# Optimization experiments

Measured on AMD Instinct MI355X. Metric: run time of the kernel, lower is better.

The kernel has to match this reference:

```python
import jax, jax.numpy as jnp
import numpy as np

N, E, D_IN, D_OUT, R, B = 50000, 800000, 64, 64, 10, 4

def setup_inputs() -> dict:
    key = jax.random.key(0)
    ks = jax.random.split(key, 8)
    feat = jax.random.normal(ks[0], (N, D_IN), jnp.float32)
    src = jax.random.randint(ks[1], (E,), 0, N)
    dst = jax.random.randint(ks[2], (E,), 0, N)
    etype = jax.random.randint(ks[3], (E,), 0, R)
    norm = jax.random.uniform(ks[4], (E,), jnp.float32)
    weight = jax.random.normal(ks[5], (B, D_IN, D_OUT), jnp.float32) * 0.1
    w_comp = jax.random.normal(ks[6], (R, B), jnp.float32) * 0.1
    self_loop_weight = jax.random.normal(ks[7], (D_IN, D_OUT), jnp.float32) * 0.1
    return dict(feat=feat, src=src, dst=dst, etype=etype, norm=norm,
                weight=weight, w_comp=w_comp, self_loop_weight=self_loop_weight)

def reference(feat, src, dst, etype, norm, weight, w_comp, self_loop_weight):
    # Basis decomposition: per-relation weight W_r = sum_b w_comp[r,b] * weight[b]
    W = jnp.einsum('rb,bio->rio', w_comp, weight)            # [R, D_in, D_out]
    # Transform all nodes under every relation (R is small), then gather per edge.
    # This avoids materializing an [E, D_in, D_out] per-edge weight tensor.
    xr = jnp.einsum('ni,rio->rno', feat, W)                  # [R, N, D_out]
    msg = xr[etype, src] * norm[:, None]                     # [E, D_out]
    # Scatter-aggregate messages into destination nodes (DGL sum aggregator).
    agg = jax.ops.segment_sum(msg, dst, num_segments=N)      # [N, D_out]
    # SumAggregator adds curr_emb = dst_feat @ self_loop_weight to the msg sum.
    h = feat @ self_loop_weight + agg                        # [N, D_out]
    return jax.nn.relu(h)
```

## Files before the change

### kernel.cpp

```cpp
#include <hip/hip_runtime.h>
#include <hip/hip_bf16.h>
#include <stdint.h>

#define NN 50000
#define EE 800000
#define DD 64
#define RR 10
#define BB 4
#define NPAD 50176
#define NBKT 391
#define TBLK 4301
#define BBLK 196
#define PADCAP 8192
#define FCAP 4096

using u16 = unsigned short;
using u32 = unsigned int;

typedef short v8s __attribute__((ext_vector_type(8)));
typedef float v4f __attribute__((ext_vector_type(4)));

__device__ __forceinline__ u32 f2bf_rn(float x) {
    u32 u = __float_as_uint(x);
    return (u + 0x7FFFu + ((u >> 16) & 1u)) >> 16;
}
__device__ __forceinline__ u32 pack2bf(float a, float b) {
    return f2bf_rn(a) | (f2bf_rn(b) << 16);
}

__global__ __launch_bounds__(256, 2)
void k_big(const float* __restrict__ feat,
           const float* __restrict__ weight,
           const float* __restrict__ w_comp,
           const float* __restrict__ self_w,
           const int* __restrict__ src, const int* __restrict__ dst,
           const int* __restrict__ etype, const float* __restrict__ norm,
           int* __restrict__ bcur, int* __restrict__ flag,
           uint2* __restrict__ rec,
           u16* __restrict__ xr, float* __restrict__ out,
           int nbin, int tb_off, int cap) {
    __shared__ __align__(16) char smem[34816];
    const int t = threadIdx.x;

    if ((int)blockIdx.x < nbin) {
        int* lh  = (int*)smem;
        int* gb  = lh + 392;
        int* lcc = gb + 392;
        const int ebase = (int)blockIdx.x * 4096;
        for (int b = t; b < 392; b += 256) { lh[b] = 0; lcc[b] = 0; }
        __syncthreads();
        #pragma unroll 4
        for (int j = 0; j < 16; ++j) {
            int e = ebase + t + 256 * j;
            if (e < EE) atomicAdd(&lh[dst[e] >> 7], 1);
        }
        __syncthreads();
        for (int b = t; b < 392; b += 256) {
            int c = lh[b];
            gb[b] = c ? atomicAdd(&bcur[b], c) : 0;
        }
        __syncthreads();
        #pragma unroll 4
        for (int j = 0; j < 16; ++j) {
            int e = ebase + t + 256 * j;
            if (e < EE) {
                int d = dst[e];
                int b = d >> 7;
                int p = atomicAdd(&lcc[b], 1);
                u32 w0 = (u32)src[e] | ((u32)etype[e] << 16) | ((u32)(d & 127) << 20);
                if (cap) {
                    int il = gb[b] + p;
                    if (il < cap)
                        rec[(size_t)b * cap + il] = make_uint2(w0, __float_as_uint(norm[e]));
                    else
                        atomicOr(&flag[b], 2);
                } else {
                    rec[gb[b] + p] = make_uint2(w0, __float_as_uint(norm[e]));
                }
            }
        }
        return;
    }

    u16*   sWt = (u16*)smem;
    u16*   sFb = (u16*)(smem + 9216);
    float* sD  = (float*)smem;

    const int tb = (int)blockIdx.x - nbin + tb_off;
    const int r = tb / 391;
    const int nbase = (tb % 391) * 128;

    if (r < RR) {
        const float c0 = w_comp[r * BB + 0];
        const float c1 = w_comp[r * BB + 1];
        const float c2 = w_comp[r * BB + 2];
        const float c3 = w_comp[r * BB + 3];
        #pragma unroll
        for (int qq = 0; qq < 16; ++qq) {
            int idx = t + 256 * qq;
            int n = idx & 63, k = idx >> 6;
            float v = c0 * weight[k * 64 + n] + c1 * weight[4096 + k * 64 + n] +
                      c2 * weight[8192 + k * 64 + n] + c3 * weight[12288 + k * 64 + n];
            sWt[n * 72 + k] = (u16)f2bf_rn(v);
        }
    } else {
        #pragma unroll
        for (int qq = 0; qq < 16; ++qq) {
            int idx = t + 256 * qq;
            int n = idx & 63, k = idx >> 6;
            sWt[n * 72 + k] = (u16)f2bf_rn(self_w[k * 64 + n]);
        }
    }

    #pragma unroll
    for (int qq = 0; qq < 8; ++qq) {
        int f4 = qq * 256 + t;
        int nl = f4 >> 4;
        int ic = (f4 & 15) << 2;
        int n = nbase + nl;
        float4 v = make_float4(0.f, 0.f, 0.f, 0.f);
        if (n < NN) v = reinterpret_cast<const float4*>(feat)[(size_t)n * 16 + (f4 & 15)];
        *reinterpret_cast<uint2*>(&sFb[nl * 72 + ic]) =
            make_uint2(pack2bf(v.x, v.y), pack2bf(v.z, v.w));
    }
    __syncthreads();

    const int wv = t >> 6;
    const int L = t & 63;
    const int q = L >> 4;
    const int c = L & 15;

    v8s bf[4][2];
    #pragma unroll
    for (int nt = 0; nt < 4; ++nt)
        #pragma unroll
        for (int kh = 0; kh < 2; ++kh)
            bf[nt][kh] = *reinterpret_cast<const v8s*>(&sWt[(nt * 16 + c) * 72 + kh * 32 + q * 8]);

    v8s af[2][2];
    #pragma unroll
    for (int mt = 0; mt < 2; ++mt) {
        int row = wv * 32 + mt * 16 + c;
        #pragma unroll
        for (int kh = 0; kh < 2; ++kh)
            af[mt][kh] = *reinterpret_cast<const v8s*>(&sFb[row * 72 + kh * 32 + q * 8]);
    }
    __syncthreads();

    v4f acc[2][4];
    #pragma unroll
    for (int mt = 0; mt < 2; ++mt)
        #pragma unroll
        for (int nt = 0; nt < 4; ++nt) {
            acc[mt][nt] = (v4f)(0.f);
            #pragma unroll
            for (int kh = 0; kh < 2; ++kh)
                acc[mt][nt] = __builtin_amdgcn_mfma_f32_16x16x32_bf16(
                    af[mt][kh], bf[nt][kh], acc[mt][nt], 0, 0, 0);
        }

    #pragma unroll
    for (int mt = 0; mt < 2; ++mt) {
        int mrow = wv * 32 + mt * 16 + q * 4;
        #pragma unroll
        for (int nt = 0; nt < 4; ++nt)
            #pragma unroll
            for (int rg = 0; rg < 4; ++rg)
                sD[(mrow + rg) * 68 + nt * 16 + c] = acc[mt][nt][rg];
    }
    __syncthreads();

    const int row = t >> 1;
    const int cb = (t & 1) * 32;
    const int g = nbase + row;
    if (g < NN) {
        const float* sp = &sD[row * 68 + cb];
        if (r < RR) {
            u16* dp = xr + ((size_t)r * NN + g) * DD + cb;
            #pragma unroll
            for (int j = 0; j < 4; ++j) {
                float4 f0 = *reinterpret_cast<const float4*>(sp + j * 8);
                float4 f1 = *reinterpret_cast<const float4*>(sp + j * 8 + 4);
                uint4 o;
                o.x = pack2bf(f0.x, f0.y);
                o.y = pack2bf(f0.z, f0.w);
                o.z = pack2bf(f1.x, f1.y);
                o.w = pack2bf(f1.z, f1.w);
                *reinterpret_cast<uint4*>(dp + j * 8) = o;
            }
        } else {
            float* dp = out + (size_t)g * DD + cb;
            #pragma unroll
            for (int j = 0; j < 8; ++j)
                *reinterpret_cast<float4*>(dp + j * 4) =
                    *reinterpret_cast<const float4*>(sp + j * 4);
        }
    }
}

__global__ __launch_bounds__(256)
void k_bhist(const int* __restrict__ dst, int* __restrict__ bktcnt) {
    __shared__ int lh[NBKT];
    const int t = threadIdx.x;
    for (int b = t; b < NBKT; b += 256) lh[b] = 0;
    __syncthreads();
    const int ebase = blockIdx.x * 8192;
    #pragma unroll
    for (int j = 0; j < 32; ++j) {
        int e = ebase + t + 256 * j;
        if (e < EE) atomicAdd(&lh[dst[e] >> 7], 1);
    }
    __syncthreads();
    for (int b = t; b < NBKT; b += 256) {
        int v = lh[b];
        if (v) atomicAdd(&bktcnt[b], v);
    }
}

__global__ __launch_bounds__(512)
void k_bscan(const int* __restrict__ bktcnt, int* __restrict__ bktbase,
             int* __restrict__ bcur, int* __restrict__ flag) {
    __shared__ int s[512];
    int t = threadIdx.x;
    int v = (t < NBKT) ? bktcnt[t] : 0;
    s[t] = v;
    __syncthreads();
    #pragma unroll
    for (int off = 1; off < 512; off <<= 1) {
        int x = (t >= off) ? s[t - off] : 0;
        __syncthreads();
        s[t] += x;
        __syncthreads();
    }
    if (t < 392) {
        int b = s[t] - v;
        bktbase[t] = b;
        bcur[t] = b;
        flag[t] = 0;
    }
}

__global__ __launch_bounds__(512)
void k_sortb2(const int* __restrict__ bcurF, const int* __restrict__ bktbase,
              int* __restrict__ flag, uint2* __restrict__ rec,
              int* __restrict__ base, int* __restrict__ cnt, int cap) {
    __shared__ uint2 buf[PADCAP];
    __shared__ int h[128];
    __shared__ int pc[128];
    __shared__ int sc[128];
    __shared__ int lc[128];
    __shared__ int totp;
    const int b = blockIdx.x;
    const int t = threadIdx.x;
    const int seg0 = cap ? b * cap : bktbase[b];
    const int cnt_b = cap ? bcurF[b] : (bcurF[b] - seg0);
    if (flag[b] & 2) return;
    if (cnt_b > 6144) {
        if (t == 0) flag[b] = 1;
        return;
    }
    if (t < 128) h[t] = 0;
    __syncthreads();
    for (int k = t; k < cnt_b; k += 512)
        atomicAdd(&h[(rec[seg0 + k].x >> 20) & 127], 1);
    __syncthreads();
    if (t < 128) {
        pc[t] = cap ? ((h[t] + 15) & ~15) : h[t];
        sc[t] = pc[t];
    }
    __syncthreads();
    #pragma unroll
    for (int off = 1; off < 128; off <<= 1) {
        int x = 0;
        if (t < 128 && t >= off) x = sc[t - off];
        __syncthreads();
        if (t < 128) sc[t] += x;
        __syncthreads();
    }
    if (t == 127) totp = sc[127];
    __syncthreads();
    const int total = totp;
    if (total > PADCAP || (cap && total > cap)) {
        if (t == 0) flag[b] = 1;
        return;
    }
    if (t < 128) {
        int ex = sc[t] - pc[t];
        lc[t] = ex;
        base[b * 128 + t] = seg0 + ex;
        cnt[b * 128 + t] = pc[t];
    }
    for (int k = t; k < total; k += 512) buf[k] = make_uint2(0u, 0u);
    __syncthreads();
    for (int k = t; k < cnt_b; k += 512) {
        uint2 rr = rec[seg0 + k];
        int p = atomicAdd(&lc[(rr.x >> 20) & 127], 1);
        buf[p] = rr;
    }
    __syncthreads();
    for (int k = t; k < total; k += 512)
        rec[seg0 + k] = buf[k];
}

__global__ __launch_bounds__(256)
void k_agg(const int* __restrict__ base, const int* __restrict__ cnt,
           const uint2* __restrict__ rec, const u16* __restrict__ xr,
           const int* __restrict__ flag, const int* __restrict__ bktbase,
           const int* __restrict__ bcurF,
           const int* __restrict__ src, const int* __restrict__ dst,
           const int* __restrict__ etype, const float* __restrict__ norm,
           int cap, float* __restrict__ out) {
    int n = (blockIdx.x * 256 + threadIdx.x) >> 6;
    int L = threadIdx.x & 63;
    if (n >= NN) return;
    const int g = L >> 4;
    const int c = L & 15;
    float a0 = 0.f, a1 = 0.f, a2 = 0.f, a3 = 0.f;
    const int fb = flag[n >> 7];

    if (__builtin_expect(fb == 0, 1)) {
        int st = base[n];
        int cn = cnt[n];
        int k = 0;
        for (; k + 16 <= cn; k += 16) {
            uint2 r0 = rec[st + k + g];
            uint2 r1 = rec[st + k + 4 + g];
            uint2 r2 = rec[st + k + 8 + g];
            uint2 r3 = rec[st + k + 12 + g];
            size_t w0 = ((size_t)((r0.x >> 16) & 0xFu) * NN + (r0.x & 0xFFFFu)) * DD;
            size_t w1 = ((size_t)((r1.x >> 16) & 0xFu) * NN + (r1.x & 0xFFFFu)) * DD;
            size_t w2 = ((size_t)((r2.x >> 16) & 0xFu) * NN + (r2.x & 0xFFFFu)) * DD;
            size_t w3 = ((size_t)((r3.x >> 16) & 0xFu) * NN + (r3.x & 0xFFFFu)) * DD;
            uint2 u0 = *reinterpret_cast<const uint2*>(&xr[w0 + 4 * c]);
            uint2 u1 = *reinterpret_cast<const uint2*>(&xr[w1 + 4 * c]);
            uint2 u2 = *reinterpret_cast<const uint2*>(&xr[w2 + 4 * c]);
            uint2 u3 = *reinterpret_cast<const uint2*>(&xr[w3 + 4 * c]);
            float n0 = __uint_as_float(r0.y), n1 = __uint_as_float(r1.y);
            float n2 = __uint_as_float(r2.y), n3 = __uint_as_float(r3.y);
            a0 = fmaf(__uint_as_float((u0.x & 0xFFFFu) << 16), n0, a0);
            a1 = fmaf(__uint_as_float(u0.x & 0xFFFF0000u), n0, a1);
            a2 = fmaf(__uint_as_float((u0.y & 0xFFFFu) << 16), n0, a2);
            a3 = fmaf(__uint_as_float(u0.y & 0xFFFF0000u), n0, a3);
            a0 = fmaf(__uint_as_float((u1.x & 0xFFFFu) << 16), n1, a0);
            a1 = fmaf(__uint_as_float(u1.x & 0xFFFF0000u), n1, a1);
            a2 = fmaf(__uint_as_float((u1.y & 0xFFFFu) << 16), n1, a2);
            a3 = fmaf(__uint_as_float(u1.y & 0xFFFF0000u), n1, a3);
            a0 = fmaf(__uint_as_float((u2.x & 0xFFFFu) << 16), n2, a0);
            a1 = fmaf(__uint_as_float(u2.x & 0xFFFF0000u), n2, a1);
            a2 = fmaf(__uint_as_float((u2.y & 0xFFFFu) << 16), n2, a2);
            a3 = fmaf(__uint_as_float(u2.y & 0xFFFF0000u), n2, a3);
            a0 = fmaf(__uint_as_float((u3.x & 0xFFFFu) << 16), n3, a0);
            a1 = fmaf(__uint_as_float(u3.x & 0xFFFF0000u), n3, a1);
            a2 = fmaf(__uint_as_float((u3.y & 0xFFFFu) << 16), n3, a2);
            a3 = fmaf(__uint_as_float(u3.y & 0xFFFF0000u), n3, a3);
        }
        for (int kk = k + g; kk < cn; kk += 4) {
            uint2 rr = rec[st + kk];
            size_t rw = ((size_t)((rr.x >> 16) & 0xFu) * NN + (rr.x & 0xFFFFu)) * DD;
            uint2 u = *reinterpret_cast<const uint2*>(&xr[rw + 4 * c]);
            float nm = __uint_as_float(rr.y);
            a0 = fmaf(__uint_as_float((u.x & 0xFFFFu) << 16), nm, a0);
            a1 = fmaf(__uint_as_float(u.x & 0xFFFF0000u), nm, a1);
            a2 = fmaf(__uint_as_float((u.y & 0xFFFFu) << 16), nm, a2);
            a3 = fmaf(__uint_as_float(u.y & 0xFFFF0000u), nm, a3);
        }
    } else if (fb & 2) {
        for (int e = g; e < EE; e += 4) {
            if (dst[e] == n) {
                size_t rw = ((size_t)etype[e] * NN + src[e]) * DD;
                uint2 u = *reinterpret_cast<const uint2*>(&xr[rw + 4 * c]);
                float nm = norm[e];
                a0 = fmaf(__uint_as_float((u.x & 0xFFFFu) << 16), nm, a0);
                a1 = fmaf(__uint_as_float(u.x & 0xFFFF0000u), nm, a1);
                a2 = fmaf(__uint_as_float((u.y & 0xFFFFu) << 16), nm, a2);
                a3 = fmaf(__uint_as_float(u.y & 0xFFFF0000u), nm, a3);
            }
        }
    } else {
        int b = n >> 7;
        int seg0 = cap ? b * cap : bktbase[b];
        int segend = cap ? (b * cap + bcurF[b]) : bcurF[b];
        int my = n & 127;
        for (int k = seg0 + g; k < segend; k += 4) {
            uint2 rr = rec[k];
            if (((rr.x >> 20) & 127) == (u32)my) {
                size_t rw = ((size_t)((rr.x >> 16) & 0xFu) * NN + (rr.x & 0xFFFFu)) * DD;
                uint2 u = *reinterpret_cast<const uint2*>(&xr[rw + 4 * c]);
                float nm = __uint_as_float(rr.y);
                a0 = fmaf(__uint_as_float((u.x & 0xFFFFu) << 16), nm, a0);
                a1 = fmaf(__uint_as_float(u.x & 0xFFFF0000u), nm, a1);
                a2 = fmaf(__uint_as_float((u.y & 0xFFFFu) << 16), nm, a2);
                a3 = fmaf(__uint_as_float(u.y & 0xFFFF0000u), nm, a3);
            }
        }
    }
    a0 += __shfl_xor(a0, 16); a1 += __shfl_xor(a1, 16);
    a2 += __shfl_xor(a2, 16); a3 += __shfl_xor(a3, 16);
    a0 += __shfl_xor(a0, 32); a1 += __shfl_xor(a1, 32);
    a2 += __shfl_xor(a2, 32); a3 += __shfl_xor(a3, 32);
    if (g == 0) {
        size_t o = (size_t)n * DD + 4 * c;
        float4 v = *reinterpret_cast<const float4*>(&out[o]);
        v.x = fmaxf(v.x + a0, 0.f);
        v.y = fmaxf(v.y + a1, 0.f);
        v.z = fmaxf(v.z + a2, 0.f);
        v.w = fmaxf(v.w + a3, 0.f);
        *reinterpret_cast<float4*>(&out[o]) = v;
    }
}

__global__ __launch_bounds__(256)
void k_edges(const int* __restrict__ src, const int* __restrict__ dst,
             const int* __restrict__ etype, const float* __restrict__ norm,
             const u16* __restrict__ xr, float* __restrict__ out) {
    int gtid = blockIdx.x * 256 + threadIdx.x;
    int e = gtid >> 4;
    int l = gtid & 15;
    if (e >= EE) return;
    int s = src[e];
    int d = dst[e];
    int rt = etype[e];
    float nm = norm[e];
    size_t row = ((size_t)rt * NN + s) * DD;
    uint2 u = *reinterpret_cast<const uint2*>(&xr[row + l * 4]);
    float f0 = __uint_as_float((u.x & 0xFFFFu) << 16);
    float f1 = __uint_as_float(u.x & 0xFFFF0000u);
    float f2 = __uint_as_float((u.y & 0xFFFFu) << 16);
    float f3 = __uint_as_float(u.y & 0xFFFF0000u);
    float* op = out + (size_t)d * DD + l * 4;
    atomicAdd(op + 0, f0 * nm);
    atomicAdd(op + 1, f1 * nm);
    atomicAdd(op + 2, f2 * nm);
    atomicAdd(op + 3, f3 * nm);
}

__global__ void k_makeW(const float* __restrict__ weight,
                        const float* __restrict__ w_comp,
                        float* __restrict__ W) {
    int f = blockIdx.x * 256 + threadIdx.x;
    if (f >= RR * 4096) return;
    int r = f >> 12;
    int io = f & 4095;
    float v = 0.f;
    #pragma unroll
    for (int b = 0; b < BB; ++b) v += w_comp[r * BB + b] * weight[b * 4096 + io];
    W[f] = v;
}

__global__ __launch_bounds__(256)
void k_edges_direct(const int* __restrict__ src, const int* __restrict__ dst,
                    const int* __restrict__ etype, const float* __restrict__ norm,
                    const float* __restrict__ feat, const float* __restrict__ W,
                    float* __restrict__ out) {
    int gtid = blockIdx.x * 256 + threadIdx.x;
    int e = gtid >> 6;
    int lane = gtid & 63;
    if (e >= EE) return;
    int s = src[e];
    int d = dst[e];
    int rt = etype[e];
    float nm = norm[e];
    const float* fr = feat + (size_t)s * DD;
    const float* Wr = W + (size_t)rt * 4096;
    float acc = 0.f;
    #pragma unroll
    for (int i = 0; i < DD; ++i) acc = fmaf(fr[i], Wr[i * DD + lane], acc);
    atomicAdd(&out[(size_t)d * DD + lane], acc * nm);
}

__global__ __launch_bounds__(256)
void k_relu(float* __restrict__ out) {
    int i = blockIdx.x * 256 + threadIdx.x;
    float4* p = reinterpret_cast<float4*>(out);
    float4 v = p[i];
    v.x = fmaxf(v.x, 0.f);
    v.y = fmaxf(v.y, 0.f);
    v.z = fmaxf(v.z, 0.f);
    v.w = fmaxf(v.w, 0.f);
    p[i] = v;
}

extern "C" void kernel_launch(void* const* d_in, const int* in_sizes, int n_in,
                              void* d_out, int out_size, void* d_ws, size_t ws_size,
                              hipStream_t stream) {
    const float* feat   = (const float*)d_in[0];
    const int*   src    = (const int*)d_in[1];
    const int*   dst    = (const int*)d_in[2];
    const int*   etype  = (const int*)d_in[3];
    const float* norm   = (const float*)d_in[4];
    const float* weight = (const float*)d_in[5];
    const float* w_comp = (const float*)d_in[6];
    const float* self_w = (const float*)d_in[7];
    float* out = (float*)d_out;

    const size_t sz_xr     = (size_t)RR * NN * DD * sizeof(u16);
    const size_t off_bkc   = sz_xr;
    const size_t off_bkb   = off_bkc + 1600;
    const size_t off_bcur  = off_bkb + 1600;
    const size_t off_flag  = off_bcur + 1600;
    const size_t off_base  = off_flag + 1600;
    const size_t off_cnt   = off_base + (size_t)NPAD * 4;
    const size_t off_rec   = off_cnt + (size_t)NPAD * 4;
    const size_t need_hist  = off_rec + (size_t)EE * 8;
    const size_t need_fixed = off_rec + (size_t)NBKT * FCAP * 8;

    dim3 blk(256);
    char* ws = (char*)d_ws;

    if (ws_size >= need_hist) {
        u16*  xr      = (u16*)ws;
        int*  bktcnt  = (int*)(ws + off_bkc);
        int*  bktbase = (int*)(ws + off_bkb);
        int*  bcur    = (int*)(ws + off_bcur);
        int*  flag    = (int*)(ws + off_flag);
        int*  basep   = (int*)(ws + off_base);
        int*  cntp    = (int*)(ws + off_cnt);
        uint2* rec    = (uint2*)(ws + off_rec);
        const int cap = (ws_size >= need_fixed) ? FCAP : 0;

        hipMemsetAsync(bktcnt, 0, 6400, stream);
        if (!cap) {
            k_bhist<<<dim3(98), blk, 0, stream>>>(dst, bktcnt);
            k_bscan<<<dim3(1), dim3(512), 0, stream>>>(bktcnt, bktbase, bcur, flag);
        }
        k_big<<<dim3(TBLK + BBLK), blk, 0, stream>>>(feat, weight, w_comp, self_w,
                                                     src, dst, etype, norm,
                                                     bcur, flag, rec, xr, out,
                                                     BBLK, 0, cap);
        k_sortb2<<<dim3(NBKT), dim3(512), 0, stream>>>(bcur, bktbase, flag, rec,
                                                       basep, cntp, cap);
        k_agg<<<dim3((NN * 64 + 255) / 256), blk, 0, stream>>>(
            basep, cntp, rec, xr, flag, bktbase, bcur,
            src, dst, etype, norm, cap, out);
    } else if (ws_size >= sz_xr) {
        u16* xr = (u16*)d_ws;
        k_big<<<dim3(TBLK), blk, 0, stream>>>(feat, weight, w_comp, self_w,
                                              src, dst, etype, norm,
                                              (int*)d_ws, (int*)d_ws, (uint2*)d_ws,
                                              xr, out, 0, 0, 0);
        k_edges<<<dim3(EE * 16 / 256), blk, 0, stream>>>(src, dst, etype, norm, xr, out);
        k_relu<<<dim3(NN * DD / 4 / 256), blk, 0, stream>>>(out);
    } else {
        k_big<<<dim3(391), blk, 0, stream>>>(feat, weight, w_comp, self_w,
                                             src, dst, etype, norm,
                                             (int*)d_ws, (int*)d_ws, (uint2*)d_ws,
                                             (u16*)d_ws, out, 0, 3910, 0);
        float* W = (float*)d_ws;
        k_makeW<<<dim3(160), blk, 0, stream>>>(weight, w_comp, W);
        k_edges_direct<<<dim3(EE * 64 / 256), blk, 0, stream>>>(src, dst, etype, norm,
                                                                feat, W, out);
        k_relu<<<dim3(NN * DD / 4 / 256), blk, 0, stream>>>(out);
    }
}
```

Measured before the change: 168.2 us.

## Fuse bucket sort into big kernel with spin-wait, loop relations per tile

The per-bucket sort kernel is folded into k_big as a third block role. Those blocks spin on a global counter of finished binning blocks before sorting each bucket in shared memory, which removes one kernel launch. Transform blocks now process one node tile across all relations, loading the features once and rebuilding the relation weight per iteration, so there are far fewer blocks. The spin-wait relies on the binning blocks being scheduled first and on forward progress, and the larger shared-memory footprint lowers occupancy.

```diff
diff --git a/kernel.cpp b/kernel.cpp
--- a/kernel.cpp
+++ b/kernel.cpp
@@ -9,9 +9,9 @@
 #define BB 4
 #define NPAD 50176
 #define NBKT 391
-#define TBLK 4301
+#define NTILE 391
 #define BBLK 196
-#define PADCAP 8192
+#define PADCAP 6144
 #define FCAP 4096
 
 using u16 = unsigned short;
@@ -36,17 +36,19 @@
            const int* __restrict__ src, const int* __restrict__ dst,
            const int* __restrict__ etype, const float* __restrict__ norm,
            int* __restrict__ bcur, int* __restrict__ flag,
-           uint2* __restrict__ rec,
-           u16* __restrict__ xr, float* __restrict__ out,
-           int nbin, int tb_off, int cap) {
-    __shared__ __align__(16) char smem[34816];
+           int* __restrict__ bin_done, const int* __restrict__ bktbase,
+           uint2* __restrict__ rec, u16* __restrict__ xr, float* __restrict__ out,
+           int* __restrict__ basep, int* __restrict__ cntp,
+           int nbin, int r0, int cap) {
+    __shared__ __align__(16) char smem[62464];
     const int t = threadIdx.x;
-
-    if ((int)blockIdx.x < nbin) {
+    const int bid = (int)blockIdx.x;
+
+    if (bid < nbin) {
         int* lh  = (int*)smem;
         int* gb  = lh + 392;
         int* lcc = gb + 392;
-        const int ebase = (int)blockIdx.x * 4096;
+        const int ebase = bid * 4096;
         for (int b = t; b < 392; b += 256) { lh[b] = 0; lcc[b] = 0; }
         __syncthreads();
         #pragma unroll 4
@@ -79,122 +81,195 @@
                 }
             }
         }
+        __threadfence();
+        __syncthreads();
+        if (t == 0) atomicAdd(bin_done, 1);
         return;
     }
 
-    u16*   sWt = (u16*)smem;
-    u16*   sFb = (u16*)(smem + 9216);
-    float* sD  = (float*)smem;
-
-    const int tb = (int)blockIdx.x - nbin + tb_off;
-    const int r = tb / 391;
-    const int nbase = (tb % 391) * 128;
-
-    if (r < RR) {
-        const float c0 = w_comp[r * BB + 0];
-        const float c1 = w_comp[r * BB + 1];
-        const float c2 = w_comp[r * BB + 2];
-        const float c3 = w_comp[r * BB + 3];
+    if (bid < nbin + NTILE) {
+        u16*   sWt = (u16*)smem;
+        float* sD  = (float*)(smem + 9216);
+        u16*   sFb = (u16*)(smem + 44032);
+        const int tile = bid - nbin;
+        const int nbase = tile * 128;
+
         #pragma unroll
-        for (int qq = 0; qq < 16; ++qq) {
-            int idx = t + 256 * qq;
-            int n = idx & 63, k = idx >> 6;
-            float v = c0 * weight[k * 64 + n] + c1 * weight[4096 + k * 64 + n] +
-                      c2 * weight[8192 + k * 64 + n] + c3 * weight[12288 + k * 64 + n];
-            sWt[n * 72 + k] = (u16)f2bf_rn(v);
-        }
-    } else {
+        for (int qq = 0; qq < 8; ++qq) {
+            int f4 = qq * 256 + t;
+            int nl = f4 >> 4;
+            int ic = (f4 & 15) << 2;
+            int n = nbase + nl;
+            float4 v = make_float4(0.f, 0.f, 0.f, 0.f);
+            if (n < NN) v = reinterpret_cast<const float4*>(feat)[(size_t)n * 16 + (f4 & 15)];
+            *reinterpret_cast<uint2*>(&sFb[nl * 72 + ic]) =
+                make_uint2(pack2bf(v.x, v.y), pack2bf(v.z, v.w));
+        }
+        __syncthreads();
+
+        const int wv = t >> 6;
+        const int L = t & 63;
+        const int q = L >> 4;
+        const int c = L & 15;
+
+        v8s af[2][2];
         #pragma unroll
-        for (int qq = 0; qq < 16; ++qq) {
-            int idx = t + 256 * qq;
-            int n = idx & 63, k = idx >> 6;
-            sWt[n * 72 + k] = (u16)f2bf_rn(self_w[k * 64 + n]);
-        }
-    }
-
-    #pragma unroll
-    for (int qq = 0; qq < 8; ++qq) {
-        int f4 = qq * 256 + t;
-        int nl = f4 >> 4;
-        int ic = (f4 & 15) << 2;
-        int n = nbase + nl;
-        float4 v = make_float4(0.f, 0.f, 0.f, 0.f);
-        if (n < NN) v = reinterpret_cast<const float4*>(feat)[(size_t)n * 16 + (f4 & 15)];
-        *reinterpret_cast<uint2*>(&sFb[nl * 72 + ic]) =
-            make_uint2(pack2bf(v.x, v.y), pack2bf(v.z, v.w));
-    }
-    __syncthreads();
-
-    const int wv = t >> 6;
-    const int L = t & 63;
-    const int q = L >> 4;
-    const int c = L & 15;
-
-    v8s bf[4][2];
-    #pragma unroll
-    for (int nt = 0; nt < 4; ++nt)
-        #pragma unroll
-        for (int kh = 0; kh < 2; ++kh)
-            bf[nt][kh] = *reinterpret_cast<const v8s*>(&sWt[(nt * 16 + c) * 72 + kh * 32 + q * 8]);
-
-    v8s af[2][2];
-    #pragma unroll
-    for (int mt = 0; mt < 2; ++mt) {
-        int row = wv * 32 + mt * 16 + c;
-        #pragma unroll
-        for (int kh = 0; kh < 2; ++kh)
-            af[mt][kh] = *reinterpret_cast<const v8s*>(&sFb[row * 72 + kh * 32 + q * 8]);
-    }
-    __syncthreads();
-
-    v4f acc[2][4];
-    #pragma unroll
-    for (int mt = 0; mt < 2; ++mt)
-        #pragma unroll
-        for (int nt = 0; nt < 4; ++nt) {
-            acc[mt][nt] = (v4f)(0.f);
+        for (int mt = 0; mt < 2; ++mt) {
+            int row = wv * 32 + mt * 16 + c;
             #pragma unroll
             for (int kh = 0; kh < 2; ++kh)
-                acc[mt][nt] = __builtin_amdgcn_mfma_f32_16x16x32_bf16(
-                    af[mt][kh], bf[nt][kh], acc[mt][nt], 0, 0, 0);
-        }
-
-    #pragma unroll
-    for (int mt = 0; mt < 2; ++mt) {
-        int mrow = wv * 32 + mt * 16 + q * 4;
+                af[mt][kh] = *reinterpret_cast<const v8s*>(&sFb[row * 72 + kh * 32 + q * 8]);
+        }
+
+        for (int r = r0; r <= RR; ++r) {
+            if (r < RR) {
+                const float c0 = w_comp[r * BB + 0];
+                const float c1 = w_comp[r * BB + 1];
+                const float c2 = w_comp[r * BB + 2];
+                const float c3 = w_comp[r * BB + 3];
+                #pragma unroll
+                for (int qq = 0; qq < 16; ++qq) {
+                    int idx = t + 256 * qq;
+                    int n = idx & 63, k = idx >> 6;
+                    float v = c0 * weight[k * 64 + n] + c1 * weight[4096 + k * 64 + n] +
+                              c2 * weight[8192 + k * 64 + n] + c3 * weight[12288 + k * 64 + n];
+                    sWt[n * 72 + k] = (u16)f2bf_rn(v);
+                }
+            } else {
+                #pragma unroll
+                for (int qq = 0; qq < 16; ++qq) {
+                    int idx = t + 256 * qq;
+                    int n = idx & 63, k = idx >> 6;
+                    sWt[n * 72 + k] = (u16)f2bf_rn(self_w[k * 64 + n]);
+                }
+            }
+            __syncthreads();
+
+            v8s bfr[4][2];
+            #pragma unroll
+            for (int nt = 0; nt < 4; ++nt)
+                #pragma unroll
+                for (int kh = 0; kh < 2; ++kh)
+                    bfr[nt][kh] = *reinterpret_cast<const v8s*>(
+                        &sWt[(nt * 16 + c) * 72 + kh * 32 + q * 8]);
+
+            v4f acc[2][4];
+            #pragma unroll
+            for (int mt = 0; mt < 2; ++mt)
+                #pragma unroll
+                for (int nt = 0; nt < 4; ++nt) {
+                    acc[mt][nt] = (v4f)(0.f);
+                    #pragma unroll
+                    for (int kh = 0; kh < 2; ++kh)
+                        acc[mt][nt] = __builtin_amdgcn_mfma_f32_16x16x32_bf16(
+                            af[mt][kh], bfr[nt][kh], acc[mt][nt], 0, 0, 0);
+                }
+
+            #pragma unroll
+            for (int mt = 0; mt < 2; ++mt) {
+                int mrow = wv * 32 + mt * 16 + q * 4;
+                #pragma unroll
+                for (int nt = 0; nt < 4; ++nt)
+                    #pragma unroll
+                    for (int rg = 0; rg < 4; ++rg)
+                        sD[(mrow + rg) * 68 + nt * 16 + c] = acc[mt][nt][rg];
+            }
+            __syncthreads();
+
+            const int row2 = t >> 1;
+            const int cb = (t & 1) * 32;
+            const int g = nbase + row2;
+            if (g < NN) {
+                const float* sp = &sD[row2 * 68 + cb];
+                if (r < RR) {
+                    u16* dp = xr + ((size_t)r * NN + g) * DD + cb;
+                    #pragma unroll
+                    for (int j = 0; j < 4; ++j) {
+                        float4 f0 = *reinterpret_cast<const float4*>(sp + j * 8);
+                        float4 f1 = *reinterpret_cast<const float4*>(sp + j * 8 + 4);
+                        uint4 o;
+                        o.x = pack2bf(f0.x, f0.y);
+                        o.y = pack2bf(f0.z, f0.w);
+                        o.z = pack2bf(f1.x, f1.y);
+                        o.w = pack2bf(f1.z, f1.w);
+                        *reinterpret_cast<uint4*>(dp + j * 8) = o;
+                    }
+                } else {
+                    float* dp = out + (size_t)g * DD + cb;
+                    #pragma unroll
+                    for (int j = 0; j < 8; ++j)
+                        *reinterpret_cast<float4*>(dp + j * 4) =
+                            *reinterpret_cast<const float4*>(sp + j * 4);
+                }
+            }
+        }
+        return;
+    }
+
+    {
+        uint2* buf = (uint2*)smem;
+        int* h  = (int*)(smem + 49152);
+        int* pc = h + 128;
+        int* sc = pc + 128;
+        int* lc = sc + 128;
+        int* totp = lc + 128;
+        const int b = bid - nbin - NTILE;
+        if (t == 0) {
+            while (__hip_atomic_load(bin_done, __ATOMIC_ACQUIRE,
+                                     __HIP_MEMORY_SCOPE_AGENT) < nbin)
+                __builtin_amdgcn_s_sleep(8);
+        }
+        __syncthreads();
+        __threadfence();
+
+        const int seg0 = cap ? b * cap : bktbase[b];
+        const int cnt_b = cap ? bcur[b] : (bcur[b] - seg0);
+        if (flag[b] & 2) return;
+        if (cnt_b > PADCAP) {
+            if (t == 0) flag[b] = 1;
+            return;
+        }
+        if (t < 128) h[t] = 0;
+        __syncthreads();
+        for (int k = t; k < cnt_b; k += 256)
+            atomicAdd(&h[(rec[seg0 + k].x >> 20) & 127], 1);
+        __syncthreads();
+        if (t < 128) {
+            pc[t] = cap ? ((h[t] + 15) & ~15) : h[t];
+            sc[t] = pc[t];
+        }
+        __syncthreads();
         #pragma unroll
-        for (int nt = 0; nt < 4; ++nt)
-            #pragma unroll
-            for (int rg = 0; rg < 4; ++rg)
-                sD[(mrow + rg) * 68 + nt * 16 + c] = acc[mt][nt][rg];
-    }
-    __syncthreads();
-
-    const int row = t >> 1;
-    const int cb = (t & 1) * 32;
-    const int g = nbase + row;
-    if (g < NN) {
-        const float* sp = &sD[row * 68 + cb];
-        if (r < RR) {
-            u16* dp = xr + ((size_t)r * NN + g) * DD + cb;
-            #pragma unroll
-            for (int j = 0; j < 4; ++j) {
-                float4 f0 = *reinterpret_cast<const float4*>(sp + j * 8);
-                float4 f1 = *reinterpret_cast<const float4*>(sp + j * 8 + 4);
-                uint4 o;
-                o.x = pack2bf(f0.x, f0.y);
-                o.y = pack2bf(f0.z, f0.w);
-                o.z = pack2bf(f1.x, f1.y);
-                o.w = pack2bf(f1.z, f1.w);
-                *reinterpret_cast<uint4*>(dp + j * 8) = o;
-            }
-        } else {
-            float* dp = out + (size_t)g * DD + cb;
-            #pragma unroll
-            for (int j = 0; j < 8; ++j)
-                *reinterpret_cast<float4*>(dp + j * 4) =
-                    *reinterpret_cast<const float4*>(sp + j * 4);
-        }
+        for (int off = 1; off < 128; off <<= 1) {
+            int x = 0;
+            if (t < 128 && t >= off) x = sc[t - off];
+            __syncthreads();
+            if (t < 128) sc[t] += x;
+            __syncthreads();
+        }
+        if (t == 127) *totp = sc[127];
+        __syncthreads();
+        const int total = *totp;
+        if (total > PADCAP || (cap && total > cap)) {
+            if (t == 0) flag[b] = 1;
+            return;
+        }
+        if (t < 128) {
+            int ex = sc[t] - pc[t];
+            lc[t] = ex;
+            basep[b * 128 + t] = seg0 + ex;
+            cntp[b * 128 + t] = pc[t];
+        }
+        for (int k = t; k < total; k += 256) buf[k] = make_uint2(0u, 0u);
+        __syncthreads();
+        for (int k = t; k < cnt_b; k += 256) {
+            uint2 rr = rec[seg0 + k];
+            int p = atomicAdd(&lc[(rr.x >> 20) & 127], 1);
+            buf[p] = rr;
+        }
+        __syncthreads();
+        for (int k = t; k < total; k += 256)
+            rec[seg0 + k] = buf[k];
     }
 }
 
@@ -238,68 +313,6 @@
         bcur[t] = b;
         flag[t] = 0;
     }
-}
-
-__global__ __launch_bounds__(512)
-void k_sortb2(const int* __restrict__ bcurF, const int* __restrict__ bktbase,
-              int* __restrict__ flag, uint2* __restrict__ rec,
-              int* __restrict__ base, int* __restrict__ cnt, int cap) {
-    __shared__ uint2 buf[PADCAP];
-    __shared__ int h[128];
-    __shared__ int pc[128];
-    __shared__ int sc[128];
-    __shared__ int lc[128];
-    __shared__ int totp;
-    const int b = blockIdx.x;
-    const int t = threadIdx.x;
-    const int seg0 = cap ? b * cap : bktbase[b];
-    const int cnt_b = cap ? bcurF[b] : (bcurF[b] - seg0);
-    if (flag[b] & 2) return;
-    if (cnt_b > 6144) {
-        if (t == 0) flag[b] = 1;
-        return;
-    }
-    if (t < 128) h[t] = 0;
-    __syncthreads();
-    for (int k = t; k < cnt_b; k += 512)
-        atomicAdd(&h[(rec[seg0 + k].x >> 20) & 127], 1);
-    __syncthreads();
-    if (t < 128) {
-        pc[t] = cap ? ((h[t] + 15) & ~15) : h[t];
-        sc[t] = pc[t];
-    }
-    __syncthreads();
-    #pragma unroll
-    for (int off = 1; off < 128; off <<= 1) {
-        int x = 0;
-        if (t < 128 && t >= off) x = sc[t - off];
-        __syncthreads();
-        if (t < 128) sc[t] += x;
-        __syncthreads();
-    }
-    if (t == 127) totp = sc[127];
-    __syncthreads();
-    const int total = totp;
-    if (total > PADCAP || (cap && total > cap)) {
-        if (t == 0) flag[b] = 1;
-        return;
-    }
-    if (t < 128) {
-        int ex = sc[t] - pc[t];
-        lc[t] = ex;
-        base[b * 128 + t] = seg0 + ex;
-        cnt[b * 128 + t] = pc[t];
-    }
-    for (int k = t; k < total; k += 512) buf[k] = make_uint2(0u, 0u);
-    __syncthreads();
-    for (int k = t; k < cnt_b; k += 512) {
-        uint2 rr = rec[seg0 + k];
-        int p = atomicAdd(&lc[(rr.x >> 20) & 127], 1);
-        buf[p] = rr;
-    }
-    __syncthreads();
-    for (int k = t; k < total; k += 512)
-        rec[seg0 + k] = buf[k];
 }
 
 __global__ __launch_bounds__(256)
@@ -493,14 +506,15 @@
     const float* self_w = (const float*)d_in[7];
     float* out = (float*)d_out;
 
-    const size_t sz_xr     = (size_t)RR * NN * DD * sizeof(u16);
-    const size_t off_bkc   = sz_xr;
-    const size_t off_bkb   = off_bkc + 1600;
-    const size_t off_bcur  = off_bkb + 1600;
-    const size_t off_flag  = off_bcur + 1600;
-    const size_t off_base  = off_flag + 1600;
-    const size_t off_cnt   = off_base + (size_t)NPAD * 4;
-    const size_t off_rec   = off_cnt + (size_t)NPAD * 4;
+    const size_t sz_xr    = (size_t)RR * NN * DD * sizeof(u16);
+    const size_t off_bkc  = sz_xr;
+    const size_t off_bkb  = off_bkc + 1600;
+    const size_t off_bcur = off_bkb + 1600;
+    const size_t off_flag = off_bcur + 1600;
+    const size_t off_done = off_flag + 1600;
+    const size_t off_base = off_done + 64;
+    const size_t off_cnt  = off_base + (size_t)NPAD * 4;
+    const size_t off_rec  = off_cnt + (size_t)NPAD * 4;
     const size_t need_hist  = off_rec + (size_t)EE * 8;
     const size_t need_fixed = off_rec + (size_t)NBKT * FCAP * 8;
 
@@ -513,38 +527,39 @@
         int*  bktbase = (int*)(ws + off_bkb);
         int*  bcur    = (int*)(ws + off_bcur);
         int*  flag    = (int*)(ws + off_flag);
+        int*  bdone   = (int*)(ws + off_done);
         int*  basep   = (int*)(ws + off_base);
         int*  cntp    = (int*)(ws + off_cnt);
         uint2* rec    = (uint2*)(ws + off_rec);
         const int cap = (ws_size >= need_fixed) ? FCAP : 0;
 
-        hipMemsetAsync(bktcnt, 0, 6400, stream);
+        hipMemsetAsync(bktcnt, 0, 6464, stream);
         if (!cap) {
             k_bhist<<<dim3(98), blk, 0, stream>>>(dst, bktcnt);
             k_bscan<<<dim3(1), dim3(512), 0, stream>>>(bktcnt, bktbase, bcur, flag);
         }
-        k_big<<<dim3(TBLK + BBLK), blk, 0, stream>>>(feat, weight, w_comp, self_w,
-                                                     src, dst, etype, norm,
-                                                     bcur, flag, rec, xr, out,
-                                                     BBLK, 0, cap);
-        k_sortb2<<<dim3(NBKT), dim3(512), 0, stream>>>(bcur, bktbase, flag, rec,
-                                                       basep, cntp, cap);
+        k_big<<<dim3(BBLK + NTILE + NBKT), blk, 0, stream>>>(
+            feat, weight, w_comp, self_w, src, dst, etype, norm,
+            bcur, flag, bdone, bktbase, rec, xr, out, basep, cntp,
+            BBLK, 0, cap);
         k_agg<<<dim3((NN * 64 + 255) / 256), blk, 0, stream>>>(
             basep, cntp, rec, xr, flag, bktbase, bcur,
             src, dst, etype, norm, cap, out);
     } else if (ws_size >= sz_xr) {
         u16* xr = (u16*)d_ws;
-        k_big<<<dim3(TBLK), blk, 0, stream>>>(feat, weight, w_comp, self_w,
-                                              src, dst, etype, norm,
-                                              (int*)d_ws, (int*)d_ws, (uint2*)d_ws,
-                                              xr, out, 0, 0, 0);
+        k_big<<<dim3(NTILE), blk, 0, stream>>>(
+            feat, weight, w_comp, self_w, src, dst, etype, norm,
+            (int*)d_ws, (int*)d_ws, (int*)d_ws, (int*)d_ws,
+            (uint2*)d_ws, xr, out, (int*)d_ws, (int*)d_ws,
+            0, 0, 0);
         k_edges<<<dim3(EE * 16 / 256), blk, 0, stream>>>(src, dst, etype, norm, xr, out);
         k_relu<<<dim3(NN * DD / 4 / 256), blk, 0, stream>>>(out);
     } else {
-        k_big<<<dim3(391), blk, 0, stream>>>(feat, weight, w_comp, self_w,
-                                             src, dst, etype, norm,
-                                             (int*)d_ws, (int*)d_ws, (uint2*)d_ws,
-                                             (u16*)d_ws, out, 0, 3910, 0);
+        k_big<<<dim3(NTILE), blk, 0, stream>>>(
+            feat, weight, w_comp, self_w, src, dst, etype, norm,
+            (int*)d_ws, (int*)d_ws, (int*)d_ws, (int*)d_ws,
+            (uint2*)d_ws, (u16*)d_ws, out, (int*)d_ws, (int*)d_ws,
+            0, RR, 0);
         float* W = (float*)d_ws;
         k_makeW<<<dim3(160), blk, 0, stream>>>(weight, w_comp, W);
         k_edges_direct<<<dim3(EE * 64 / 256), blk, 0, stream>>>(src, dst, etype, norm,
```

Result: slower. 282.3 us (+67.8%).
